# Kernel optimization log

Hardware: AMD Instinct MI355X
Metric: run time of the kernel (lower is better)

## Reference

```python
import jax, jax.numpy as jnp
import numpy as np
from jax import lax

V, E, H = 90000, 256, 512  # vocab, embed_dim, lstm_dim
B, TE, TD = 16, 64, 32     # batch, encoder time, decoder time
NEG = jnp.float32(-1e9)


def setup_inputs() -> dict:
    key = jax.random.key(0)
    ks = jax.random.split(key, 16)
    u = lambda k, shape, s: jax.random.uniform(k, shape, jnp.float32, -s, s)
    inp = {
        "encoder_inputs": jax.random.randint(ks[0], (B, TE), 0, V, dtype=jnp.int32),
        "decoder_inputs": jax.random.randint(ks[1], (B, TD), 0, V, dtype=jnp.int32),
        "encoder_lengths": jnp.maximum(jax.random.randint(ks[2], (B,), 1, TE + 1, dtype=jnp.int32), 1),
        "decoder_lengths": jnp.maximum(jax.random.randint(ks[3], (B,), 1, TD + 1, dtype=jnp.int32), 1),
        "embeddings": u(ks[4], (V, E), 1.0 / 16),
        # encoder BasicLSTMCell: kernel [E+H, 4H], bias [4H]
        "W_enc": u(ks[5], (E + H, 4 * H), 1.0 / np.sqrt(E + H)),
        "b_enc": jnp.zeros((4 * H,), jnp.float32),
        # decoder cell input = concat(embed, attention[H]) -> kernel [(E+H)+H, 4H]
        "W_dec": u(ks[6], (E + 2 * H, 4 * H), 1.0 / np.sqrt(E + 2 * H)),
        "b_dec": jnp.zeros((4 * H,), jnp.float32),
        # Bahdanau attention: memory layer, query layer, score vector v
        "W_mem": u(ks[7], (H, H), 1.0 / np.sqrt(H)),
        "W_query": u(ks[8], (H, H), 1.0 / np.sqrt(H)),
        "v_att": u(ks[9], (H,), 1.0 / np.sqrt(H)),
        # attention_layer: Dense(H, use_bias=False) on concat(cell_out, context)
        "W_attn": u(ks[10], (2 * H, H), 1.0 / np.sqrt(2 * H)),
        # output projection: Dense(90000, use_bias=False)
        "W_proj": u(ks[11], (H, V), 1.0 / np.sqrt(H)),
    }
    return inp


def _lstm_step(x, h, c, W, b):
    # TF BasicLSTMCell: gates i, j, f, o; forget_bias = 1.0
    z = jnp.concatenate([x, h], axis=-1) @ W + b
    i, j, f, o = jnp.split(z, 4, axis=-1)
    c2 = c * jax.nn.sigmoid(f + 1.0) + jax.nn.sigmoid(i) * jnp.tanh(j)
    h2 = jnp.tanh(c2) * jax.nn.sigmoid(o)
    return h2, c2


def reference(encoder_inputs, decoder_inputs, encoder_lengths, decoder_lengths,
              embeddings, W_enc, b_enc, W_dec, b_dec,
              W_mem, W_query, v_att, W_attn, W_proj):
    q_emb = embeddings[encoder_inputs]  # [B,TE,E]
    r_emb = embeddings[decoder_inputs]  # [B,TD,E]
    zeros_h = jnp.zeros((B, H), jnp.float32)

    # ---- encoder: dynamic_rnn semantics (zero outputs / frozen state past length)
    def enc_step(carry, xs):
        c, h = carry
        x_t, t = xs
        h2, c2 = _lstm_step(x_t, h, c, W_enc, b_enc)
        valid = (t < encoder_lengths)[:, None]
        h2 = jnp.where(valid, h2, h)
        c2 = jnp.where(valid, c2, c)
        return (c2, h2), jnp.where(valid, h2, 0.0)

    (c_e, h_e), enc_out = lax.scan(
        enc_step, (zeros_h, zeros_h),
        (q_emb.transpose(1, 0, 2), jnp.arange(TE)))
    enc_out = enc_out.transpose(1, 0, 2)  # [B,TE,H]

    keys = jnp.einsum('bth,hk->btk', enc_out, W_mem)  # memory layer
    enc_mask = jnp.arange(TE)[None, :] < encoder_lengths[:, None]  # [B,TE]

    # ---- decoder: AttentionWrapper(LSTM) + Bahdanau attention, per step
    def dec_step(carry, xs):
        c, h, attn = carry
        x_t, t = xs
        h2, c2 = _lstm_step(jnp.concatenate([x_t, attn], axis=-1), h, c, W_dec, b_dec)
        pq = h2 @ W_query  # [B,H]
        score = jnp.einsum('h,bth->bt', v_att, jnp.tanh(keys + pq[:, None, :]))
        score = jnp.where(enc_mask, score, NEG)
        align = jax.nn.softmax(score, axis=-1)
        ctx = jnp.einsum('bt,bth->bh', align, enc_out)
        attn2 = jnp.concatenate([h2, ctx], axis=-1) @ W_attn  # attention_layer
        logits_t = attn2 @ W_proj  # [B,V]
        # dynamic_decode zeros emissions once finished (t >= decoder_length)
        logits_t = jnp.where((t < decoder_lengths)[:, None], logits_t, 0.0)
        return (c2, h2, attn2), logits_t

    # initial state: zero_state cloned with cell_state = encoder final state
    _, logits = lax.scan(
        dec_step, (c_e, h_e, zeros_h),
        (r_emb.transpose(1, 0, 2), jnp.arange(TD)))
    return logits.transpose(1, 0, 2)  # [B,TD,V]
```

## Files before the change

### kernel.cpp

```cpp
#include <hip/hip_runtime.h>

#define E_  256
#define H_  512
#define B_  16
#define TE_ 64
#define TD_ 32
#define V_  90000
#define G4_ 2048
#define NBLK_ 128

typedef __attribute__((ext_vector_type(8))) short short8;
typedef __attribute__((ext_vector_type(4))) float f32x4;
typedef _Float16 half2_ __attribute__((ext_vector_type(2)));

__device__ __forceinline__ float sigm(float x) { return 1.f / (1.f + __expf(-x)); }
__device__ __forceinline__ float tanh_(float x) {
  float e = __expf(-2.f * fabsf(x));
  float r = (1.f - e) / (1.f + e);
  return x >= 0.f ? r : -r;
}
__device__ __forceinline__ unsigned short f2bf(float v) {
  union { float f; unsigned u; } c; c.f = v;
  unsigned r = c.u + 0x7FFFu + ((c.u >> 16) & 1u);
  return (unsigned short)(r >> 16);
}
__device__ __forceinline__ unsigned pack2(float a, float b) {
  union { unsigned u; _Float16 h[2]; } p;
  p.h[0] = (_Float16)a; p.h[1] = (_Float16)b;
  return p.u;
}
__device__ __forceinline__ float dot2u(unsigned w, unsigned h, float acc) {
#if __has_builtin(__builtin_amdgcn_fdot2)
  union { unsigned u; half2_ v; } a, b; a.u = w; b.u = h;
  return __builtin_amdgcn_fdot2(a.v, b.v, acc, false);
#else
  union { unsigned u; _Float16 h[2]; } a, b; a.u = w; b.u = h;
  return acc + (float)a.h[0] * (float)b.h[0] + (float)a.h[1] * (float)b.h[1];
#endif
}
__device__ __forceinline__ float dot8(uint4 w, uint4 h, float acc) {
  acc = dot2u(w.x, h.x, acc);
  acc = dot2u(w.y, h.y, acc);
  acc = dot2u(w.z, h.z, acc);
  acc = dot2u(w.w, h.w, acc);
  return acc;
}

__device__ __forceinline__ unsigned ld_ag(const unsigned* p) {
  return __hip_atomic_load(p, __ATOMIC_RELAXED, __HIP_MEMORY_SCOPE_AGENT);
}
__device__ __forceinline__ void st_ag(unsigned* p, unsigned v) {
  __hip_atomic_store(p, v, __ATOMIC_RELAXED, __HIP_MEMORY_SCOPE_AGENT);
}

__global__ __launch_bounds__(256) void k_cv(
    const float* __restrict__ W_enc, const float* __restrict__ W_dec,
    const float* __restrict__ W_query, const float* __restrict__ W_attn,
    const float* __restrict__ W_mem,
    uint4* __restrict__ Ue, uint4* __restrict__ Ud, uint4* __restrict__ Wq,
    uint4* __restrict__ Wa, uint4* __restrict__ Wm)
{
  int u = blockIdx.x * 256 + threadIdx.x;
  const float* src; uint4* dst; int C, r0, lu;
  if (u < 131072)      { src = W_enc;   dst = Ue; C = 2048; r0 = 256; lu = u; }
  else if (u < 393216) { src = W_dec;   dst = Ud; C = 2048; r0 = 256; lu = u - 131072; }
  else if (u < 425984) { src = W_query; dst = Wq; C = 512;  r0 = 0;   lu = u - 393216; }
  else if (u < 491520) { src = W_attn;  dst = Wa; C = 512;  r0 = 0;   lu = u - 425984; }
  else                 { src = W_mem;   dst = Wm; C = 512;  r0 = 0;   lu = u - 491520; }
  int kc = lu / C, col = lu - kc * C;
  union { uint4 v; _Float16 h[8]; } p;
  #pragma unroll
  for (int e = 0; e < 8; ++e)
    p.h[e] = (_Float16)src[(size_t)(r0 + kc * 8 + e) * C + col];
  dst[(size_t)kc * C + col] = p.v;
}

__global__ __launch_bounds__(256) void k_xg(
    const int* __restrict__ toks, const float* __restrict__ emb,
    const float* __restrict__ W, const float* __restrict__ bias,
    float* __restrict__ Xg)
{
  const int tid = threadIdx.x;
  const int cc = tid & 63;
  const int tg = tid >> 6;
  const int col = blockIdx.x * 64 + cc;
  const int t0 = blockIdx.y * 64 + tg * 16;
  const float* ep[16];
  #pragma unroll
  for (int i = 0; i < 16; ++i) ep[i] = emb + (size_t)toks[t0 + i] * E_;
  float acc[16];
  float bv = bias[col];
  #pragma unroll
  for (int i = 0; i < 16; ++i) acc[i] = bv;
  for (int k4 = 0; k4 < 64; ++k4) {
    float w0 = W[(size_t)(k4 * 4 + 0) * G4_ + col];
    float w1 = W[(size_t)(k4 * 4 + 1) * G4_ + col];
    float w2 = W[(size_t)(k4 * 4 + 2) * G4_ + col];
    float w3 = W[(size_t)(k4 * 4 + 3) * G4_ + col];
    #pragma unroll
    for (int i = 0; i < 16; ++i) {
      float4 e4 = *(const float4*)(ep[i] + k4 * 4);
      acc[i] += e4.x * w0 + e4.y * w1 + e4.z * w2 + e4.w * w3;
    }
  }
  #pragma unroll
  for (int i = 0; i < 16; ++i)
    Xg[(size_t)(t0 + i) * G4_ + col] = acc[i];
}

__device__ __forceinline__ void gbar_lite(unsigned* bar, unsigned gen) {
  __syncthreads();
  if (threadIdx.x == 0) {
    asm volatile("s_waitcnt vmcnt(0) lgkmcnt(0)" ::: "memory");
    __hip_atomic_fetch_add(bar, 1u, __ATOMIC_RELAXED, __HIP_MEMORY_SCOPE_AGENT);
    const unsigned tgt = gen * (unsigned)NBLK_;
    while (__hip_atomic_load(bar, __ATOMIC_RELAXED, __HIP_MEMORY_SCOPE_AGENT) < tgt)
      __builtin_amdgcn_s_sleep(1);
  }
  __syncthreads();
}
__device__ __forceinline__ void gbar_heavy(unsigned* bar, unsigned gen) {
  __syncthreads();
  if (threadIdx.x == 0) {
    __threadfence();
    __hip_atomic_fetch_add(bar, 1u, __ATOMIC_RELAXED, __HIP_MEMORY_SCOPE_AGENT);
    const unsigned tgt = gen * (unsigned)NBLK_;
    while (__hip_atomic_load(bar, __ATOMIC_RELAXED, __HIP_MEMORY_SCOPE_AGENT) < tgt)
      __builtin_amdgcn_s_sleep(1);
    __threadfence();
  }
  __syncthreads();
}

__global__ __launch_bounds__(512) void k_seq(
    const int* __restrict__ enc_len, const float* __restrict__ v_att,
    const float* __restrict__ Xge, const float* __restrict__ Xgd,
    const uint4* __restrict__ Ue, const uint4* __restrict__ Ud,
    const uint4* __restrict__ WqG, const uint4* __restrict__ WaG,
    const uint4* __restrict__ WmG,
    float* __restrict__ keys, unsigned* __restrict__ enc_f16,
    unsigned* __restrict__ hbuf, unsigned* __restrict__ abuf,
    unsigned short* __restrict__ attn_bf, unsigned* __restrict__ bar)
{
  __shared__ __align__(16) uint4 sU[128 * 16];
  __shared__ __align__(16) uint4 sE[64 * 16];
  __shared__ __align__(16) uint4 sI[128 * 16];
  __shared__ __align__(16) unsigned sHC[512];
  __shared__ float pacc[256];
  __shared__ float shx[4][16];
  __shared__ float shy[4][16];
  __shared__ float pqL[512];
  __shared__ float vlL[512];
  __shared__ float atf[512];
  __shared__ float scp[64][8];
  __shared__ float al64[64];
  __shared__ float ctp[256][2];

  const int tid = threadIdx.x, bid = blockIdx.x;
  const int tlo = tid & 255, hi = tid >> 8;
  const int b = tlo & 15, g = (tlo >> 4) & 3, hcl = tlo >> 6;
  const int wl = hcl * 4 + g;
  const int el = enc_len[b];
  const int elB = (bid < 16) ? enc_len[bid] : 0;
  unsigned gen = 0;
  unsigned* const hb0 = hbuf;
  unsigned* const hb1 = hbuf + 4096;
  unsigned* sIu = (unsigned*)sI;

  for (int idx = tid; idx < 64 * 16; idx += 512) {
    int kc = idx >> 4, w = idx & 15;
    sE[idx] = Ue[(size_t)kc * 2048 + (w & 3) * 512 + bid * 4 + (w >> 2)];
  }
  for (int idx = tid; idx < 128 * 16; idx += 512) {
    int kc = idx >> 4, w = idx & 15;
    sU[idx] = Ud[(size_t)kc * 2048 + (w & 3) * 512 + bid * 4 + (w >> 2)];
  }
  if (tid < 32) st_ag(abuf + bid * 32 + tid, 0u);
  if (bid < 16) vlL[tid] = v_att[tid];

  float c = 0.f, hreg = 0.f;
  const uint4* ef4 = (const uint4*)enc_f16;

  for (int t = 0; t < TE_; ++t) {
    unsigned* hb_prev = (t & 1) ? hb0 : hb1;
    unsigned* hb_cur  = (t & 1) ? hb1 : hb0;
    if (t == 0) {
      for (int idx = tid; idx < 4096; idx += 512) sIu[idx] = 0u;
    } else {
      for (int idx = tid; idx < 4096; idx += 512) {
        int w = idx & 3, bb = (idx >> 2) & 15, kc = idx >> 6;
        sIu[idx] = ld_ag(hb_prev + bb * 256 + kc * 4 + w);
      }
    }
    __syncthreads();
    float acc;
    {
      const int kc0 = hi ? 32 : 0;
      acc = hi ? 0.f
               : Xge[(size_t)(b * TE_ + t) * G4_ + g * 512 + bid * 4 + hcl];
      const uint4* wp = sE + kc0 * 16 + wl;
      const uint4* ip = sI + kc0 * 16 + b;
      #pragma unroll 4
      for (int kc = 0; kc < 32; ++kc)
        acc = dot8(wp[kc * 16], ip[kc * 16], acc);
    }
    if (hi) pacc[tlo] = acc;
    __syncthreads();
    if (!hi) {
      acc += pacc[tlo];
      float v0 = acc;
      float v1 = __shfl_xor(v0, 16);
      float v2 = __shfl_xor(v0, 32);
      float v3 = __shfl_xor(v0, 48);
      float gi = (g == 0) ? v0 : (g == 1) ? v1 : (g == 2) ? v2 : v3;
      float gj = (g == 0) ? v1 : (g == 1) ? v0 : (g == 2) ? v3 : v2;
      float gf = (g == 0) ? v2 : (g == 1) ? v3 : (g == 2) ? v0 : v1;
      float go = (g == 0) ? v3 : (g == 1) ? v2 : (g == 2) ? v1 : v0;
      float c2 = c * sigm(gf + 1.f) + sigm(gi) * tanh_(gj);
      float h2 = tanh_(c2) * sigm(go);
      bool valid = t < el;
      c = valid ? c2 : c;
      hreg = valid ? h2 : hreg;
      if (g == 0) {
        shx[hcl][b] = hreg;
        shy[hcl][b] = valid ? h2 : 0.f;
      }
    }
    __syncthreads();
    if (tid < 32) {
      int bb = tid & 15, pr = tid >> 4;
      st_ag(hb_cur + bb * 256 + bid * 2 + pr, pack2(shx[2 * pr][bb], shx[2 * pr + 1][bb]));
      enc_f16[(size_t)(bb * TE_ + t) * 256 + bid * 2 + pr] =
          pack2(shy[2 * pr][bb], shy[2 * pr + 1][bb]);
    }
    ++gen;
    if (t == TE_ - 1) gbar_heavy(bar, gen);
    else              gbar_lite(bar, gen);
  }

  {
    for (int idx = tid; idx < 8 * 64; idx += 512) {
      int r = idx >> 6, kc = idx & 63;
      sI[idx] = ef4[(size_t)(bid * 8 + r) * 64 + kc];
    }
    __syncthreads();
    float a8[8] = {0.f, 0.f, 0.f, 0.f, 0.f, 0.f, 0.f, 0.f};
    const uint4* wm = WmG + tid;
    for (int kc = 0; kc < 64; ++kc) {
      uint4 w = wm[(size_t)kc * 512];
      #pragma unroll
      for (int r = 0; r < 8; ++r) a8[r] = dot8(w, sI[r * 64 + kc], a8[r]);
    }
    #pragma unroll
    for (int r = 0; r < 8; ++r)
      keys[(size_t)(bid * 8 + r) * 512 + tid] = a8[r];
    ++gen; gbar_heavy(bar, gen);
  }

  for (int t = 0; t < TD_; ++t) {
    unsigned* hb_prev = (t & 1) ? hb0 : hb1;
    unsigned* hb_cur  = (t & 1) ? hb1 : hb0;
    for (int idx = tid; idx < 8192; idx += 512) {
      int w = idx & 3, bb = (idx >> 2) & 15, kc = idx >> 6;
      sIu[idx] = (kc < 64) ? ld_ag(abuf + bb * 256 + kc * 4 + w)
                           : ld_ag(hb_prev + bb * 256 + (kc - 64) * 4 + w);
    }
    __syncthreads();
    float acc;
    {
      const int kc0 = hi ? 64 : 0;
      acc = hi ? 0.f
               : Xgd[(size_t)(b * TD_ + t) * G4_ + g * 512 + bid * 4 + hcl];
      const uint4* wp = sU + kc0 * 16 + wl;
      const uint4* ip = sI + kc0 * 16 + b;
      #pragma unroll 4
      for (int kc = 0; kc < 64; ++kc)
        acc = dot8(wp[kc * 16], ip[kc * 16], acc);
    }
    if (hi) pacc[tlo] = acc;
    __syncthreads();
    if (!hi) {
      acc += pacc[tlo];
      float v0 = acc;
      float v1 = __shfl_xor(v0, 16);
      float v2 = __shfl_xor(v0, 32);
      float v3 = __shfl_xor(v0, 48);
      float gi = (g == 0) ? v0 : (g == 1) ? v1 : (g == 2) ? v2 : v3;
      float gj = (g == 0) ? v1 : (g == 1) ? v0 : (g == 2) ? v3 : v2;
      float gf = (g == 0) ? v2 : (g == 1) ? v3 : (g == 2) ? v0 : v1;
      float go = (g == 0) ? v3 : (g == 1) ? v2 : (g == 2) ? v1 : v0;
      float c2 = c * sigm(gf + 1.f) + sigm(gi) * tanh_(gj);
      float h2 = tanh_(c2) * sigm(go);
      c = c2;
      if (g == 0) shx[hcl][b] = h2;
    }
    __syncthreads();
    if (tid < 32) {
      int bb = tid & 15, pr = tid >> 4;
      st_ag(hb_cur + bb * 256 + bid * 2 + pr, pack2(shx[2 * pr][bb], shx[2 * pr + 1][bb]));
    }
    ++gen; gbar_lite(bar, gen);

    if (bid < 16) {
      if (tid < 256) sHC[tid] = ld_ag(hb_cur + bid * 256 + tid);
      __syncthreads();
      {
        float a = 0.f;
        const uint4* hv = (const uint4*)sHC;
        const uint4* wq = WqG + tid;
        #pragma unroll 4
        for (int kc = 0; kc < 64; ++kc)
          a = dot8(wq[(size_t)kc * 512], hv[kc], a);
        pqL[tid] = a;
      }
      __syncthreads();
      {
        int tt = tid >> 3, q = tid & 7;
        const float4* kr = (const float4*)(keys + (size_t)(bid * TE_ + tt) * 512 + q * 64);
        const float4* pp = (const float4*)(pqL + q * 64);
        const float4* vp = (const float4*)(vlL + q * 64);
        float s = 0.f;
        #pragma unroll 4
        for (int i = 0; i < 16; ++i) {
          float4 k4 = kr[i], p4 = pp[i], v4 = vp[i];
          s += v4.x * tanh_(k4.x + p4.x) + v4.y * tanh_(k4.y + p4.y)
             + v4.z * tanh_(k4.z + p4.z) + v4.w * tanh_(k4.w + p4.w);
        }
        scp[tt][q] = s;
      }
      __syncthreads();
      if (tid < 64) {
        float sum = 0.f;
        #pragma unroll
        for (int q = 0; q < 8; ++q) sum += scp[tid][q];
        float sc = (tid < elB) ? sum : -1e9f;
        float m = sc;
        for (int o = 32; o > 0; o >>= 1) m = fmaxf(m, __shfl_xor(m, o));
        float p = __expf(sc - m);
        float l = p;
        for (int o = 32; o > 0; o >>= 1) l += __shfl_xor(l, o);
        al64[tid] = p / l;
      }
      __syncthreads();
      {
        const int j = tlo;
        float c0 = 0.f, c1 = 0.f;
        const unsigned* eb = enc_f16 + (size_t)(bid * TE_ + hi * 32) * 256 + j;
        #pragma unroll 8
        for (int t2 = 0; t2 < 32; ++t2) {
          union { unsigned u; _Float16 h[2]; } u2;
          u2.u = eb[(size_t)t2 * 256];
          float a = al64[hi * 32 + t2];
          c0 += a * (float)u2.h[0];
          c1 += a * (float)u2.h[1];
        }
        if (hi) { ctp[j][0] = c0; ctp[j][1] = c1; }
        __syncthreads();
        if (!hi)
          sHC[256 + j] = pack2(c0 + ctp[j][0], c1 + ctp[j][1]);
        __syncthreads();
      }
      {
        float a = 0.f;
        const uint4* iv2 = (const uint4*)sHC;
        const uint4* wa = WaG + tid;
        #pragma unroll 2
        for (int kc = 0; kc < 128; ++kc)
          a = dot8(wa[(size_t)kc * 512], iv2[kc], a);
        attn_bf[(size_t)(bid * TD_ + t) * 512 + tid] = f2bf(a);
        atf[tid] = a;
      }
      __syncthreads();
      if (tid < 256) st_ag(abuf + bid * 256 + tid, pack2(atf[2 * tid], atf[2 * tid + 1]));
    }
    ++gen; gbar_lite(bar, gen);
  }
}

__global__ __launch_bounds__(512) void k_proj(
    const float* __restrict__ Wp, const unsigned short* __restrict__ Abf,
    const int* __restrict__ dec_len_g, float* __restrict__ out)
{
  __shared__ unsigned short Al[512 * 40];
  __shared__ unsigned short Bl[128 * 40];
  __shared__ int dl[16];
  const int tid = threadIdx.x;
  const int n0 = blockIdx.x * 128;
  const int wave = tid >> 6, lane = tid & 63;
  if (tid < 16) dl[tid] = dec_len_g[tid];
  f32x4 acc[4][8] = {};
  for (int kc = 0; kc < 16; ++kc) {
    const int k0 = kc * 32;
    {
      const unsigned short* src = Abf + (size_t)tid * 512 + k0;
      unsigned short* dst = Al + tid * 40;
      *(uint4*)(dst)      = *(const uint4*)(src);
      *(uint4*)(dst + 8)  = *(const uint4*)(src + 8);
      *(uint4*)(dst + 16) = *(const uint4*)(src + 16);
      *(uint4*)(dst + 24) = *(const uint4*)(src + 24);
    }
    {
      int kk = tid >> 4;
      int nn = (tid & 15) * 8;
      const float* src = Wp + (size_t)(k0 + kk) * V_ + n0 + nn;
      #pragma unroll
      for (int j = 0; j < 8; ++j) {
        float v = (n0 + nn + j < V_) ? src[j] : 0.f;
        Bl[(nn + j) * 40 + kk] = f2bf(v);
      }
    }
    __syncthreads();
    short8 bfr[8];
    #pragma unroll
    for (int nt = 0; nt < 8; ++nt)
      bfr[nt] = *(const short8*)&Bl[(nt * 16 + (lane & 15)) * 40 + (lane >> 4) * 8];
    #pragma unroll
    for (int mt = 0; mt < 4; ++mt) {
      short8 af = *(const short8*)&Al[(wave * 64 + mt * 16 + (lane & 15)) * 40 + (lane >> 4) * 8];
      #pragma unroll
      for (int nt = 0; nt < 8; ++nt)
        acc[mt][nt] = __builtin_amdgcn_mfma_f32_16x16x32_bf16(af, bfr[nt], acc[mt][nt], 0, 0, 0);
    }
    __syncthreads();
  }
  #pragma unroll
  for (int mt = 0; mt < 4; ++mt) {
    #pragma unroll
    for (int e = 0; e < 4; ++e) {
      int r = wave * 64 + mt * 16 + ((lane >> 4) << 2) + e;
      bool valid = (r & 31) < dl[r >> 5];
      #pragma unroll
      for (int nt = 0; nt < 8; ++nt) {
        int gcol = n0 + nt * 16 + (lane & 15);
        if (gcol < V_)
          out[(size_t)r * V_ + gcol] = valid ? acc[mt][nt][e] : 0.f;
      }
    }
  }
}

extern "C" void kernel_launch(void* const* d_in, const int* in_sizes, int n_in,
                              void* d_out, int out_size, void* d_ws, size_t ws_size,
                              hipStream_t stream) {
  const int* enc_in   = (const int*)d_in[0];
  const int* dec_in   = (const int*)d_in[1];
  const int* enc_len  = (const int*)d_in[2];
  const int* dec_len  = (const int*)d_in[3];
  const float* emb    = (const float*)d_in[4];
  const float* W_enc  = (const float*)d_in[5];
  const float* b_enc  = (const float*)d_in[6];
  const float* W_dec  = (const float*)d_in[7];
  const float* b_dec  = (const float*)d_in[8];
  const float* W_mem  = (const float*)d_in[9];
  const float* W_query= (const float*)d_in[10];
  const float* v_att  = (const float*)d_in[11];
  const float* W_attn = (const float*)d_in[12];
  const float* W_proj = (const float*)d_in[13];
  float* out = (float*)d_out;
  char* ws = (char*)d_ws;

  float* Xge          = (float*)(ws + 0);
  float* Xgd          = (float*)(ws + 8388608);
  uint4* Ue           = (uint4*)(ws + 12582912);
  uint4* Ud           = (uint4*)(ws + 14680064);
  uint4* Wq           = (uint4*)(ws + 18874368);
  uint4* Wa           = (uint4*)(ws + 19398656);
  uint4* Wm           = (uint4*)(ws + 20447232);
  unsigned* hbuf      = (unsigned*)(ws + 20971520);
  unsigned* abuf      = (unsigned*)(ws + 21004288);
  unsigned* bar       = (unsigned*)(ws + 21020672);
  unsigned* enc_f16   = (unsigned*)(ws + 23068672);
  float* keys         = (float*)(ws + 24117248);
  unsigned short* attn_bf = (unsigned short*)(ws + 26214400);

  k_cv<<<2048, 256, 0, stream>>>(W_enc, W_dec, W_query, W_attn, W_mem,
                                 Ue, Ud, Wq, Wa, Wm);
  k_xg<<<dim3(32, 16), 256, 0, stream>>>(enc_in, emb, W_enc, b_enc, Xge);
  k_xg<<<dim3(32, 8),  256, 0, stream>>>(dec_in, emb, W_dec, b_dec, Xgd);
  hipMemsetAsync(bar, 0, 64, stream);
  {
    const int* a0 = enc_len; const float* a1 = v_att;
    const float* a2 = Xge;   const float* a3 = Xgd;
    const uint4* a4 = Ue;    const uint4* a5 = Ud;
    const uint4* a6 = Wq;    const uint4* a7 = Wa;
    const uint4* a8 = Wm;
    float* a9 = keys;        unsigned* a10 = enc_f16;
    unsigned* a11 = hbuf;    unsigned* a12 = abuf;
    unsigned short* a13 = attn_bf; unsigned* a14 = bar;
    void* kargs[] = { &a0, &a1, &a2, &a3, &a4, &a5, &a6, &a7, &a8,
                      &a9, &a10, &a11, &a12, &a13, &a14 };
    hipLaunchCooperativeKernel((void*)k_seq, dim3(NBLK_), dim3(512),
                               kargs, 0, stream);
  }
  k_proj<<<704, 512, 0, stream>>>(W_proj, attn_bf, dec_len, out);
}
```

Baseline: 2.186 ms.

## Distribute decoder query and attention-layer matvecs across all blocks with flag-array barriers

The per-step query projection and attention-layer matvec used to run only in the 16 batch blocks, each streaming the full weight matrix from global memory. They now run across all 128 blocks, with each block holding its own slice of W_query and W_attn in LDS, and results pass through new global buffers (pq_g, cbuf). The atomic-counter grid barrier becomes a per-block flag array that 128 threads poll, which avoids contention on a single atomic. The cost is two extra grid barriers per decoder step and more global round-trips for exchanging partial results.

```diff
diff --git a/kernel.cpp b/kernel.cpp
--- a/kernel.cpp
+++ b/kernel.cpp
@@ -108,27 +108,28 @@
     Xg[(size_t)(t0 + i) * G4_ + col] = acc[i];
 }
 
-__device__ __forceinline__ void gbar_lite(unsigned* bar, unsigned gen) {
+__device__ __forceinline__ void gbar(unsigned* flags, unsigned gen) {
   __syncthreads();
   if (threadIdx.x == 0) {
     asm volatile("s_waitcnt vmcnt(0) lgkmcnt(0)" ::: "memory");
-    __hip_atomic_fetch_add(bar, 1u, __ATOMIC_RELAXED, __HIP_MEMORY_SCOPE_AGENT);
-    const unsigned tgt = gen * (unsigned)NBLK_;
-    while (__hip_atomic_load(bar, __ATOMIC_RELAXED, __HIP_MEMORY_SCOPE_AGENT) < tgt)
-      __builtin_amdgcn_s_sleep(1);
+    st_ag(flags + blockIdx.x, gen);
+  }
+  if (threadIdx.x < NBLK_) {
+    while (ld_ag(flags + threadIdx.x) < gen) __builtin_amdgcn_s_sleep(1);
   }
   __syncthreads();
 }
-__device__ __forceinline__ void gbar_heavy(unsigned* bar, unsigned gen) {
+__device__ __forceinline__ void gbar_heavy(unsigned* flags, unsigned gen) {
   __syncthreads();
   if (threadIdx.x == 0) {
     __threadfence();
-    __hip_atomic_fetch_add(bar, 1u, __ATOMIC_RELAXED, __HIP_MEMORY_SCOPE_AGENT);
-    const unsigned tgt = gen * (unsigned)NBLK_;
-    while (__hip_atomic_load(bar, __ATOMIC_RELAXED, __HIP_MEMORY_SCOPE_AGENT) < tgt)
-      __builtin_amdgcn_s_sleep(1);
-    __threadfence();
-  }
+    st_ag(flags + blockIdx.x, gen);
+  }
+  if (threadIdx.x < NBLK_) {
+    while (ld_ag(flags + threadIdx.x) < gen) __builtin_amdgcn_s_sleep(1);
+  }
+  __syncthreads();
+  if (threadIdx.x == 0) __threadfence();
   __syncthreads();
 }
 
@@ -140,18 +141,20 @@
     const uint4* __restrict__ WmG,
     float* __restrict__ keys, unsigned* __restrict__ enc_f16,
     unsigned* __restrict__ hbuf, unsigned* __restrict__ abuf,
+    unsigned* __restrict__ pq_g, unsigned* __restrict__ cbuf,
     unsigned short* __restrict__ attn_bf, unsigned* __restrict__ bar)
 {
   __shared__ __align__(16) uint4 sU[128 * 16];
   __shared__ __align__(16) uint4 sE[64 * 16];
   __shared__ __align__(16) uint4 sI[128 * 16];
-  __shared__ __align__(16) unsigned sHC[512];
+  __shared__ __align__(16) uint4 sQ[64 * 4];
+  __shared__ __align__(16) uint4 sA[128 * 4];
+  __shared__ float red[512];
   __shared__ float pacc[256];
   __shared__ float shx[4][16];
   __shared__ float shy[4][16];
   __shared__ float pqL[512];
   __shared__ float vlL[512];
-  __shared__ float atf[512];
   __shared__ float scp[64][8];
   __shared__ float al64[64];
   __shared__ float ctp[256][2];
@@ -174,6 +177,14 @@
   for (int idx = tid; idx < 128 * 16; idx += 512) {
     int kc = idx >> 4, w = idx & 15;
     sU[idx] = Ud[(size_t)kc * 2048 + (w & 3) * 512 + bid * 4 + (w >> 2)];
+  }
+  for (int idx = tid; idx < 64 * 4; idx += 512) {
+    int kc = idx >> 2, cl = idx & 3;
+    sQ[idx] = WqG[(size_t)kc * 512 + bid * 4 + cl];
+  }
+  for (int idx = tid; idx < 128 * 4; idx += 512) {
+    int kc = idx >> 2, cl = idx & 3;
+    sA[idx] = WaG[(size_t)kc * 512 + bid * 4 + cl];
   }
   if (tid < 32) st_ag(abuf + bid * 32 + tid, 0u);
   if (bid < 16) vlL[tid] = v_att[tid];
@@ -235,7 +246,7 @@
     }
     ++gen;
     if (t == TE_ - 1) gbar_heavy(bar, gen);
-    else              gbar_lite(bar, gen);
+    else              gbar(bar, gen);
   }
 
   {
@@ -257,13 +268,22 @@
     ++gen; gbar_heavy(bar, gen);
   }
 
+  const int ob = tid & 63, obb = ob & 15, ocl = ob >> 4, oseg = tid >> 6;
   for (int t = 0; t < TD_; ++t) {
     unsigned* hb_prev = (t & 1) ? hb0 : hb1;
     unsigned* hb_cur  = (t & 1) ? hb1 : hb0;
-    for (int idx = tid; idx < 8192; idx += 512) {
-      int w = idx & 3, bb = (idx >> 2) & 15, kc = idx >> 6;
-      sIu[idx] = (kc < 64) ? ld_ag(abuf + bb * 256 + kc * 4 + w)
-                           : ld_ag(hb_prev + bb * 256 + (kc - 64) * 4 + w);
+
+    if (t == 0) {
+      for (int idx = tid; idx < 8192; idx += 512) {
+        int w = idx & 3, bb = (idx >> 2) & 15, kc = idx >> 6;
+        sIu[idx] = (kc < 64) ? ld_ag(abuf + bb * 256 + kc * 4 + w)
+                             : ld_ag(hb_prev + bb * 256 + (kc - 64) * 4 + w);
+      }
+    } else {
+      for (int idx = tid; idx < 4096; idx += 512) {
+        int w = idx & 3, bb = (idx >> 2) & 15, kc = idx >> 6;
+        sIu[idx] = ld_ag(abuf + bb * 256 + kc * 4 + w);
+      }
     }
     __syncthreads();
     float acc;
@@ -299,20 +319,33 @@
       int bb = tid & 15, pr = tid >> 4;
       st_ag(hb_cur + bb * 256 + bid * 2 + pr, pack2(shx[2 * pr][bb], shx[2 * pr + 1][bb]));
     }
-    ++gen; gbar_lite(bar, gen);
+    ++gen; gbar(bar, gen);
+
+    {
+      for (int idx = tid; idx < 4096; idx += 512) {
+        int w = idx & 3, bb = (idx >> 2) & 15, kc = idx >> 6;
+        sIu[(64 + kc) * 64 + bb * 4 + w] = ld_ag(hb_cur + bb * 256 + kc * 4 + w);
+      }
+      __syncthreads();
+      float a = 0.f;
+      #pragma unroll 4
+      for (int i = 0; i < 8; ++i) {
+        int kc = oseg * 8 + i;
+        a = dot8(sQ[kc * 4 + ocl], sI[(64 + kc) * 16 + obb], a);
+      }
+      red[oseg * 64 + ob] = a;
+      __syncthreads();
+      if (tid < 64) {
+        float s = 0.f;
+        #pragma unroll
+        for (int q = 0; q < 8; ++q) s += red[q * 64 + tid];
+        st_ag(pq_g + obb * 512 + bid * 4 + ocl, __float_as_uint(s));
+      }
+    }
+    ++gen; gbar(bar, gen);
 
     if (bid < 16) {
-      if (tid < 256) sHC[tid] = ld_ag(hb_cur + bid * 256 + tid);
-      __syncthreads();
-      {
-        float a = 0.f;
-        const uint4* hv = (const uint4*)sHC;
-        const uint4* wq = WqG + tid;
-        #pragma unroll 4
-        for (int kc = 0; kc < 64; ++kc)
-          a = dot8(wq[(size_t)kc * 512], hv[kc], a);
-        pqL[tid] = a;
-      }
+      pqL[tid] = __uint_as_float(ld_ag(pq_g + bid * 512 + tid));
       __syncthreads();
       {
         int tt = tid >> 3, q = tid & 7;
@@ -357,23 +390,37 @@
         if (hi) { ctp[j][0] = c0; ctp[j][1] = c1; }
         __syncthreads();
         if (!hi)
-          sHC[256 + j] = pack2(c0 + ctp[j][0], c1 + ctp[j][1]);
-        __syncthreads();
-      }
-      {
-        float a = 0.f;
-        const uint4* iv2 = (const uint4*)sHC;
-        const uint4* wa = WaG + tid;
-        #pragma unroll 2
-        for (int kc = 0; kc < 128; ++kc)
-          a = dot8(wa[(size_t)kc * 512], iv2[kc], a);
-        attn_bf[(size_t)(bid * TD_ + t) * 512 + tid] = f2bf(a);
-        atf[tid] = a;
-      }
-      __syncthreads();
-      if (tid < 256) st_ag(abuf + bid * 256 + tid, pack2(atf[2 * tid], atf[2 * tid + 1]));
-    }
-    ++gen; gbar_lite(bar, gen);
+          st_ag(cbuf + bid * 256 + j, pack2(c0 + ctp[j][0], c1 + ctp[j][1]));
+      }
+    }
+    ++gen; gbar(bar, gen);
+
+    {
+      for (int idx = tid; idx < 4096; idx += 512) {
+        int w = idx & 3, bb = (idx >> 2) & 15, kc = idx >> 6;
+        sIu[kc * 64 + bb * 4 + w] = ld_ag(cbuf + bb * 256 + kc * 4 + w);
+      }
+      __syncthreads();
+      float a = 0.f;
+      #pragma unroll 4
+      for (int i = 0; i < 16; ++i) {
+        int kc = oseg * 16 + i;
+        int row = (kc < 64) ? (64 + kc) : (kc - 64);
+        a = dot8(sA[kc * 4 + ocl], sI[row * 16 + obb], a);
+      }
+      red[oseg * 64 + ob] = a;
+      __syncthreads();
+      if (tid < 64) {
+        float v = 0.f;
+        #pragma unroll
+        for (int q = 0; q < 8; ++q) v += red[q * 64 + tid];
+        attn_bf[(size_t)(obb * TD_ + t) * 512 + bid * 4 + ocl] = f2bf(v);
+        float vp = __shfl_xor(v, 16);
+        if (!(ocl & 1))
+          st_ag(abuf + obb * 256 + bid * 2 + (ocl >> 1), pack2(v, vp));
+      }
+    }
+    ++gen; gbar(bar, gen);
   }
 }
 
@@ -469,6 +516,8 @@
   unsigned* hbuf      = (unsigned*)(ws + 20971520);
   unsigned* abuf      = (unsigned*)(ws + 21004288);
   unsigned* bar       = (unsigned*)(ws + 21020672);
+  unsigned* pq_g      = (unsigned*)(ws + 21021696);
+  unsigned* cbuf      = (unsigned*)(ws + 21053952);
   unsigned* enc_f16   = (unsigned*)(ws + 23068672);
   float* keys         = (float*)(ws + 24117248);
   unsigned short* attn_bf = (unsigned short*)(ws + 26214400);
@@ -477,7 +526,7 @@
                                  Ue, Ud, Wq, Wa, Wm);
   k_xg<<<dim3(32, 16), 256, 0, stream>>>(enc_in, emb, W_enc, b_enc, Xge);
   k_xg<<<dim3(32, 8),  256, 0, stream>>>(dec_in, emb, W_dec, b_dec, Xgd);
-  hipMemsetAsync(bar, 0, 64, stream);
+  hipMemsetAsync(bar, 0, 1024, stream);
   {
     const int* a0 = enc_len; const float* a1 = v_att;
     const float* a2 = Xge;   const float* a3 = Xgd;
@@ -486,9 +535,10 @@
     const uint4* a8 = Wm;
     float* a9 = keys;        unsigned* a10 = enc_f16;
     unsigned* a11 = hbuf;    unsigned* a12 = abuf;
-    unsigned short* a13 = attn_bf; unsigned* a14 = bar;
+    unsigned* a13 = pq_g;    unsigned* a14 = cbuf;
+    unsigned short* a15 = attn_bf; unsigned* a16 = bar;
     void* kargs[] = { &a0, &a1, &a2, &a3, &a4, &a5, &a6, &a7, &a8,
-                      &a9, &a10, &a11, &a12, &a13, &a14 };
+                      &a9, &a10, &a11, &a12, &a13, &a14, &a15, &a16 };
     hipLaunchCooperativeKernel((void*)k_seq, dim3(NBLK_), dim3(512),
                                kargs, 0, stream);
   }
```

After: 2.258 ms. 3.3% more time.
